# Optimization experiments

Measured on AMD Instinct MI355X. Metric: run time of the kernel, lower is better.

Reference implementation:

```python
import jax, jax.numpy as jnp
import numpy as np

N_STATE = 1024
N_HEAD = 16
B, S = 2, 2048
NEG = -1e9  # finite stand-in for -inf in the additive causal mask


def setup_inputs() -> dict:
    key = jax.random.key(0)
    ks = jax.random.split(key, 8)
    sd = N_STATE ** -0.5
    x = jax.random.normal(ks[0], (B, S, N_STATE), dtype=jnp.float32)
    # additive causal mask, as in Whisper: upper triangle = -inf
    i = jnp.arange(S)
    mask = jnp.where(i[None, :] > i[:, None], NEG, 0.0).astype(jnp.float32)
    return {
        "x": x,
        "mask": mask,
        "Wq": jax.random.normal(ks[1], (N_STATE, N_STATE), jnp.float32) * sd,
        "bq": jax.random.normal(ks[2], (N_STATE,), jnp.float32) * 0.02,
        "Wk": jax.random.normal(ks[3], (N_STATE, N_STATE), jnp.float32) * sd,
        "Wv": jax.random.normal(ks[4], (N_STATE, N_STATE), jnp.float32) * sd,
        "bv": jax.random.normal(ks[5], (N_STATE,), jnp.float32) * 0.02,
        "Wo": jax.random.normal(ks[6], (N_STATE, N_STATE), jnp.float32) * sd,
        "bo": jax.random.normal(ks[7], (N_STATE,), jnp.float32) * 0.02,
    }


def reference(x, mask, Wq, bq, Wk, Wv, bv, Wo, bo):
    B_, S_, D = x.shape
    H = N_HEAD
    hd = D // H
    scale = hd ** -0.25  # applied to both q and k, per the source

    q = (x @ Wq + bq).reshape(B_, S_, H, hd) * scale   # [B,S,H,hd]
    k = (x @ Wk).reshape(B_, S_, H, hd) * scale        # key has no bias
    v = (x @ Wv + bv).reshape(B_, S_, H, hd)

    qk = jnp.einsum("bqhd,bkhd->bhqk", q, k) + mask[:S_, :S_]
    w = jax.nn.softmax(qk.astype(jnp.float32), axis=-1).astype(q.dtype)
    o = jnp.einsum("bhqk,bkhd->bqhd", w, v).reshape(B_, S_, D)
    return o @ Wo + bo
```

## Files before the change

kernel.cpp:

```cpp
#include <hip/hip_runtime.h>
#include <hip/hip_bf16.h>

#define BB 2
#define SS 2048
#define DD 1024
#define HH 16
#define HD 64
#define QKSCALE 0.35355339059327373f
#define QKSCALE_E2 0.42466090144f
#define NEGBIG (-1e9f)

using u16 = unsigned short;
typedef __attribute__((ext_vector_type(8))) short short8;
typedef __attribute__((ext_vector_type(4))) float floatx4;
typedef __attribute__((ext_vector_type(4))) unsigned short ushort4v;

#define GLOBAL_AS __attribute__((address_space(1)))
#define LDS_AS __attribute__((address_space(3)))

__device__ __forceinline__ u16 f2b(float f) {
  union { float f; unsigned u; } v; v.f = f;
  return (u16)((v.u + 0x7fffu + ((v.u >> 16) & 1u)) >> 16);
}

__device__ __forceinline__ u16 bconv(float f) {
  union { __hip_bfloat16 h; u16 u; } cv;
  cv.h = __float2bfloat16(f);
  return cv.u;
}

__device__ __forceinline__ float ex2(float f) {
  return __builtin_amdgcn_exp2f(f);
}

__device__ __forceinline__ floatx4 vmax4(floatx4 a, floatx4 b) {
  return (floatx4){fmaxf(a[0], b[0]), fmaxf(a[1], b[1]),
                   fmaxf(a[2], b[2]), fmaxf(a[3], b[3])};
}

__device__ __forceinline__ void gload_lds16(const void* g, void* l) {
  __builtin_amdgcn_global_load_lds((GLOBAL_AS void*)(g), (LDS_AS void*)(l), 16, 0, 0);
}

__global__ __launch_bounds__(256) void cvt_bf16x4(const float4* __restrict__ src,
                                                  ushort4v* __restrict__ dst, int n4) {
  int i = blockIdx.x * 256 + threadIdx.x;
  if (i >= n4) return;
  float4 f = src[i];
  ushort4v o = { f2b(f.x), f2b(f.y), f2b(f.z), f2b(f.w) };
  dst[i] = o;
}

__global__ __launch_bounds__(256) void transpose_w(const float* __restrict__ s0,
                                                   const float* __restrict__ s1,
                                                   const float* __restrict__ s2,
                                                   const float* __restrict__ s3,
                                                   u16* __restrict__ dst) {
  __shared__ float tile[32][33];
  const float* src = (blockIdx.z == 0) ? s0 : (blockIdx.z == 1) ? s1
                   : (blockIdx.z == 2) ? s2 : s3;
  u16* d = dst + (size_t)blockIdx.z * 1024 * 1024;
  int c0 = blockIdx.x * 32, r0 = blockIdx.y * 32;
  int tx = threadIdx.x, ty = threadIdx.y;
#pragma unroll
  for (int i = 0; i < 4; ++i)
    tile[ty + i * 8][tx] = src[(size_t)(r0 + ty + i * 8) * 1024 + c0 + tx];
  __syncthreads();
#pragma unroll
  for (int i = 0; i < 4; ++i)
    d[(size_t)(c0 + ty + i * 8) * 1024 + r0 + tx] = f2b(tile[tx][ty + i * 8]);
}

template <typename OutT>
__global__ __launch_bounds__(256, 3)
void gemm_bt(const u16* __restrict__ A, const u16* __restrict__ Bt,
             OutT* __restrict__ C, const float* __restrict__ bias,
             float scale, int M, int N, int K) {
  const int tid = threadIdx.x;
  const int lane = tid & 63;
  const int w = tid >> 6;
  const int id = (int)blockIdx.x;
  const int swz = (id & 7) * 64 + (id >> 3);
  const int m0 = (swz & 63) * 64;
  const int n0 = (swz >> 6) * 128;
  __shared__ u16 As[2][64 * 64];
  __shared__ u16 Bs[2][128 * 64];
  floatx4 acc[2][4];
#pragma unroll
  for (int i = 0; i < 2; ++i)
#pragma unroll
    for (int j = 0; j < 4; ++j) acc[i][j] = (floatx4){0.f, 0.f, 0.f, 0.f};

  const int wr = (w >> 1) * 32;
  const int wc = (w & 1) * 64;
  const int g = lane >> 4;
  const int lr = lane & 15;
  const size_t strideA = (size_t)K * 2;

  auto stage = [&](int k0, int buf) {
#pragma unroll
    for (int p = 0; p < 2; ++p) {
      int L = tid * 16 + p * 4096;
      int row = L >> 7;
      int cb = (L ^ ((row & 7) << 4)) & 127;
      gload_lds16((const char*)A + (size_t)(m0 + row) * strideA + k0 * 2 + cb,
                  (char*)As[buf] + p * 4096 + w * 1024);
    }
#pragma unroll
    for (int p = 0; p < 4; ++p) {
      int L = tid * 16 + p * 4096;
      int row = L >> 7;
      int cb = (L ^ ((row & 7) << 4)) & 127;
      gload_lds16((const char*)Bt + (size_t)(n0 + row) * strideA + k0 * 2 + cb,
                  (char*)Bs[buf] + p * 4096 + w * 1024);
    }
  };

  const int nsteps = K >> 6;
  stage(0, 0);
  for (int t = 0; t < nsteps; ++t) {
    const int buf = t & 1;
    __syncthreads();
    if (t + 1 < nsteps) stage((t + 1) << 6, buf ^ 1);
    const u16* as = As[buf];
    const u16* bs = Bs[buf];
#pragma unroll
    for (int ks = 0; ks < 2; ++ks) {
      short8 af[2], bf[4];
      const int c0 = ks * 32 + g * 8;
#pragma unroll
      for (int mi = 0; mi < 2; ++mi) {
        int row = wr + mi * 16 + lr;
        af[mi] = *(const short8*)(as + row * 64 + (c0 ^ ((row & 7) << 3)));
      }
#pragma unroll
      for (int ni = 0; ni < 4; ++ni) {
        int row = wc + ni * 16 + lr;
        bf[ni] = *(const short8*)(bs + row * 64 + (c0 ^ ((row & 7) << 3)));
      }
      __builtin_amdgcn_s_setprio(1);
#pragma unroll
      for (int mi = 0; mi < 2; ++mi)
#pragma unroll
        for (int ni = 0; ni < 4; ++ni)
          acc[mi][ni] = __builtin_amdgcn_mfma_f32_16x16x32_bf16(af[mi], bf[ni],
                                                                acc[mi][ni], 0, 0, 0);
      __builtin_amdgcn_s_setprio(0);
    }
  }
#pragma unroll
  for (int ni = 0; ni < 4; ++ni) {
    int col = n0 + wc + ni * 16 + lr;
    float bvv = bias ? bias[col] : 0.f;
#pragma unroll
    for (int mi = 0; mi < 2; ++mi) {
#pragma unroll
      for (int r = 0; r < 4; ++r) {
        int rowg = m0 + wr + mi * 16 + g * 4 + r;
        float val = (acc[mi][ni][r] + bvv) * scale;
        if constexpr (sizeof(OutT) == 4) C[(size_t)rowg * N + col] = val;
        else C[(size_t)rowg * N + col] = (OutT)f2b(val);
      }
    }
  }
}

__global__ __launch_bounds__(256, 4)
void gemm_qkv(const u16* __restrict__ A, const u16* __restrict__ Wt3,
              u16* __restrict__ Out3, u16* __restrict__ Vt,
              const float* __restrict__ bq, const float* __restrict__ bv) {
  const int id = (int)blockIdx.x;
  const int swz = (id & 7) * 96 + (id >> 3);
  const int bx = swz & 31;
  const int rest = swz >> 5;
  const int by = rest & 7;
  const int seg = rest >> 3;
  const u16* Bt = Wt3 + (size_t)seg * 1024 * 1024;
  u16* C = Out3 + (size_t)seg * 4096 * 1024;
  const float* bias = (seg == 0) ? bq : (seg == 2) ? bv : nullptr;
  const float scale = (seg == 2) ? 1.0f : QKSCALE_E2;

  const int tid = threadIdx.x;
  const int lane = tid & 63;
  const int w = tid >> 6;
  const int m0 = bx * 128;
  const int n0 = by * 128;
  __shared__ u16 As[2][64 * 64];
  __shared__ u16 Bs[2][64 * 64];
  floatx4 acc[4][4];
#pragma unroll
  for (int i = 0; i < 4; ++i)
#pragma unroll
    for (int j = 0; j < 4; ++j) acc[i][j] = (floatx4){0.f, 0.f, 0.f, 0.f};
  const int wr = (w >> 1) * 64;
  const int wc = (w & 1) * 64;
  const int g = lane >> 4;
  const int lr = lane & 15;

  auto stage = [&](int k0, int buf) {
#pragma unroll
    for (int p = 0; p < 2; ++p) {
      int L = tid * 16 + p * 4096;
      int lrow = L >> 7;
      int un = (L & 127) ^ ((lrow & 7) << 4);
      int r = lrow * 2 + (un >> 6);
      int cb = un & 63;
      gload_lds16((const char*)A + (size_t)(m0 + r) * 2048 + k0 * 2 + cb,
                  (char*)As[buf] + p * 4096 + w * 1024);
      gload_lds16((const char*)Bt + (size_t)(n0 + r) * 2048 + k0 * 2 + cb,
                  (char*)Bs[buf] + p * 4096 + w * 1024);
    }
  };

  stage(0, 0);
  for (int t = 0; t < 32; ++t) {
    const int buf = t & 1;
    __syncthreads();
    if (t + 1 < 32) stage((t + 1) << 5, buf ^ 1);
    const u16* as = As[buf];
    const u16* bs = Bs[buf];
    short8 af[4], bf[4];
#pragma unroll
    for (int mi = 0; mi < 4; ++mi) {
      int r = wr + mi * 16 + lr;
      af[mi] = *(const short8*)((const char*)as +
               ((r >> 1) * 128 + ((((r & 1) << 6) | (g * 16)) ^ (((r >> 1) & 7) << 4))));
    }
#pragma unroll
    for (int ni = 0; ni < 4; ++ni) {
      int r = wc + ni * 16 + lr;
      bf[ni] = *(const short8*)((const char*)bs +
               ((r >> 1) * 128 + ((((r & 1) << 6) | (g * 16)) ^ (((r >> 1) & 7) << 4))));
    }
    __builtin_amdgcn_s_setprio(1);
#pragma unroll
    for (int mi = 0; mi < 4; ++mi)
#pragma unroll
      for (int ni = 0; ni < 4; ++ni)
        acc[mi][ni] = __builtin_amdgcn_mfma_f32_16x16x32_bf16(af[mi], bf[ni],
                                                              acc[mi][ni], 0, 0, 0);
    __builtin_amdgcn_s_setprio(0);
  }

  if (seg == 2) {
    const int bseg = m0 >> 11;
    const int s0 = (m0 & 2047) + wr + g * 4;
#pragma unroll
    for (int ni = 0; ni < 4; ++ni) {
      int d = n0 + wc + ni * 16 + lr;
      float bvv = bv[d];
      u16* vrow = Vt + (size_t)(bseg * 1024 + d) * 2048;
#pragma unroll
      for (int mi = 0; mi < 4; ++mi) {
        ushort4v pk = { f2b(acc[mi][ni][0] + bvv), f2b(acc[mi][ni][1] + bvv),
                        f2b(acc[mi][ni][2] + bvv), f2b(acc[mi][ni][3] + bvv) };
        *(ushort4v*)(vrow + s0 + mi * 16) = pk;
      }
    }
    return;
  }

  __syncthreads();
  u16* eb = (w == 0) ? (u16*)As[0] : (w == 1) ? (u16*)As[1]
          : (w == 2) ? (u16*)Bs[0] : (u16*)Bs[1];
  const int rr = lane >> 2;
  const int cc = lane & 3;
  float bv4[4];
#pragma unroll
  for (int ni = 0; ni < 4; ++ni)
    bv4[ni] = bias ? bias[n0 + wc + ni * 16 + lr] : 0.f;
#pragma unroll
  for (int mi = 0; mi < 4; ++mi) {
#pragma unroll
    for (int ni = 0; ni < 4; ++ni)
#pragma unroll
      for (int r = 0; r < 4; ++r)
        eb[(g * 4 + r) * 72 + ni * 16 + lr] =
            f2b((acc[mi][ni][r] + bv4[ni]) * scale);
    short8 v0 = *(const short8*)(eb + rr * 72 + cc * 16);
    short8 v1 = *(const short8*)(eb + rr * 72 + cc * 16 + 8);
    u16* dst = C + (size_t)(m0 + wr + mi * 16 + rr) * 1024 + n0 + wc + cc * 16;
    *(short8*)dst = v0;
    *(short8*)(dst + 8) = v1;
  }
}

__device__ __forceinline__ void stream_softmax(floatx4 (&sa)[4], float& m, float& l,
                                               floatx4 (&acc)[4], u16* pl,
                                               bool diag, int wlr, int g, int lr) {
  if (diag) {
#pragma unroll
    for (int ct = 0; ct < 4; ++ct)
#pragma unroll
      for (int r = 0; r < 4; ++r)
        if (ct * 16 + g * 4 + r > wlr) sa[ct][r] += NEGBIG;
  }
  floatx4 v = vmax4(vmax4(sa[0], sa[1]), vmax4(sa[2], sa[3]));
  float mx = fmaxf(fmaxf(v[0], v[1]), fmaxf(v[2], v[3]));
  mx = fmaxf(mx, __shfl_xor(mx, 16, 64));
  mx = fmaxf(mx, __shfl_xor(mx, 32, 64));
  if (!__all(mx <= m + 8.f)) {
    float mn = fmaxf(m, mx);
    float al = ex2(m - mn);
    l *= al;
#pragma unroll
    for (int dt = 0; dt < 4; ++dt) acc[dt] *= al;
    m = mn;
  }
  floatx4 p[4];
#pragma unroll
  for (int ct = 0; ct < 4; ++ct)
#pragma unroll
    for (int r = 0; r < 4; ++r)
      p[ct][r] = ex2(sa[ct][r] - m);
  floatx4 s = (p[0] + p[1]) + (p[2] + p[3]);
  float rs = (s[0] + s[1]) + (s[2] + s[3]);
  rs += __shfl_xor(rs, 16, 64);
  rs += __shfl_xor(rs, 32, 64);
  l += rs;
#pragma unroll
  for (int ct = 0; ct < 4; ++ct) {
    ushort4v pk = { bconv(p[ct][0]), bconv(p[ct][1]),
                    bconv(p[ct][2]), bconv(p[ct][3]) };
    *(ushort4v*)((char*)pl + ((lr * 128 + ct * 32 + g * 8) ^ ((lr & 7) << 4))) = pk;
  }
}

__global__ __launch_bounds__(256, 4)
void flash_attn(const u16* __restrict__ q, const u16* __restrict__ k,
                const u16* __restrict__ vt, u16* __restrict__ o) {
  const int tid = threadIdx.x;
  const int lane = tid & 63;
  const int w = tid >> 6;
  const int g = lane >> 4;
  const int lr = lane & 15;
  const int i = (int)blockIdx.x;
  const int x = i & 7;
  const int kk = i >> 3;
  const int s = kk & 3;
  const int mI = kk >> 2;
  const int u = mI >> 3;
  const int v = mI & 7;
  const int gg = x * 4 + s;
  const int b = gg >> 4;
  const int h = gg & 15;
  const int a = (u + s) & 3;
  const int qt = (a == 0) ? v : (a == 1) ? (31 - v) : (a == 2) ? (16 + v) : (15 - v);
  const int row0 = qt * 64 + w * 16;
  const int wlr = w * 16 + lr;

  __shared__ u16 Ks[2][64 * 64];
  __shared__ u16 Vs[2][64 * 64];
  __shared__ u16 Pl[4][16 * 64];

  short8 qf[2];
  {
    const u16* qp = q + (size_t)(b * SS + row0 + lr) * DD + h * HD + g * 8;
    qf[0] = *(const short8*)qp;
    qf[1] = *(const short8*)(qp + 32);
  }
  floatx4 acc[4];
#pragma unroll
  for (int dt = 0; dt < 4; ++dt) acc[dt] = (floatx4){0.f, 0.f, 0.f, 0.f};
  float m = -1e30f, l = 0.f;

  const char* kbase = (const char*)(k + (size_t)(b * SS) * DD + h * HD);
  const char* vbase = (const char*)(vt + (size_t)((b * HH + h) * HD) * SS);
  const int nt = qt + 1;

  auto stage = [&](int t, int buf) {
    const int kvb = t * 64;
#pragma unroll
    for (int p = 0; p < 2; ++p) {
      int L = tid * 16 + p * 4096;
      int row = L >> 7;
      int cb = (L ^ ((row & 7) << 4)) & 127;
      gload_lds16(kbase + (size_t)(kvb + row) * (DD * 2) + cb,
                  (char*)Ks + buf * 8192 + p * 4096 + w * 1024);
      gload_lds16(vbase + (size_t)row * (SS * 2) + kvb * 2 + cb,
                  (char*)Vs + buf * 8192 + p * 4096 + w * 1024);
    }
  };

  stage(0, 0);
  int cur = 0;
  for (int t = 0; t < nt; ++t) {
    __syncthreads();
    if (t + 1 < nt) stage(t + 1, cur ^ 1);
    const u16* kc = Ks[cur];
    const u16* vc = Vs[cur];

    floatx4 sa[4];
#pragma unroll
    for (int ct = 0; ct < 4; ++ct) sa[ct] = (floatx4){0.f, 0.f, 0.f, 0.f};
    __builtin_amdgcn_s_setprio(1);
#pragma unroll
    for (int ks = 0; ks < 2; ++ks) {
      const int c0 = ks * 32 + g * 8;
#pragma unroll
      for (int ct = 0; ct < 4; ++ct) {
        int row = ct * 16 + lr;
        short8 kf = *(const short8*)(kc + row * 64 + (c0 ^ ((row & 7) << 3)));
        sa[ct] = __builtin_amdgcn_mfma_f32_16x16x32_bf16(kf, qf[ks], sa[ct], 0, 0, 0);
      }
    }
    __builtin_amdgcn_s_setprio(0);

    stream_softmax(sa, m, l, acc, Pl[w], t == qt, wlr, g, lr);

    __builtin_amdgcn_s_setprio(1);
#pragma unroll
    for (int ks = 0; ks < 2; ++ks) {
      const int c0 = ks * 32 + g * 8;
      int pby = (lr * 128 + ks * 64 + g * 16) ^ ((lr & 7) << 4);
      short8 pf = *(const short8*)((const char*)Pl[w] + pby);
#pragma unroll
      for (int dt = 0; dt < 4; ++dt) {
        int row = dt * 16 + lr;
        short8 vf = *(const short8*)(vc + row * 64 + (c0 ^ ((row & 7) << 3)));
        acc[dt] = __builtin_amdgcn_mfma_f32_16x16x32_bf16(vf, pf, acc[dt], 0, 0, 0);
      }
    }
    __builtin_amdgcn_s_setprio(0);
    cur ^= 1;
  }

  float inv = 1.0f / l;
#pragma unroll
  for (int dt = 0; dt < 4; ++dt) {
    ushort4v pa = { bconv(acc[dt][0] * inv), bconv(acc[dt][1] * inv),
                    bconv(acc[dt][2] * inv), bconv(acc[dt][3] * inv) };
    *(ushort4v*)(o + (size_t)(b * SS + row0 + lr) * DD + h * HD + dt * 16 + g * 4) = pa;
  }
}

extern "C" void kernel_launch(void* const* d_in, const int* in_sizes, int n_in,
                              void* d_out, int out_size, void* d_ws, size_t ws_size,
                              hipStream_t stream) {
  const float* x  = (const float*)d_in[0];
  const float* Wq = (const float*)d_in[2];
  const float* bq = (const float*)d_in[3];
  const float* Wk = (const float*)d_in[4];
  const float* Wv = (const float*)d_in[5];
  const float* bv = (const float*)d_in[6];
  const float* Wo = (const float*)d_in[7];
  const float* bo = (const float*)d_in[8];
  float* out = (float*)d_out;

  char* ws = (char*)d_ws;
  u16* xb  = (u16*)(ws);
  u16* wt  = (u16*)(ws + (8u << 20));
  u16* qkv = (u16*)(ws + (16u << 20));
  u16* vtb = (u16*)(ws + (40u << 20));
  u16* ob  = (u16*)(ws + (48u << 20));
  u16* wot = wt + 3u * 1024 * 1024;

  dim3 tb(32, 8);
  cvt_bf16x4<<<4096, 256, 0, stream>>>((const float4*)x, (ushort4v*)xb,
                                       (BB * SS * DD) / 4);
  transpose_w<<<dim3(32, 32, 4), tb, 0, stream>>>(Wq, Wk, Wv, Wo, wt);
  gemm_qkv<<<768, 256, 0, stream>>>(xb, wt, qkv, vtb, bq, bv);
  flash_attn<<<1024, 256, 0, stream>>>(qkv, qkv + (size_t)4096 * 1024, vtb, ob);
  gemm_bt<float><<<512, 256, 0, stream>>>(ob, wot, out, bo, 1.0f,
                                          4096, 1024, 1024);
}
```

Before: 109.5 us.

## Pair mirrored causal query tiles per block to share K/V staging

New measurement: 123.3 us. 1.13x slower.

```diff
diff --git a/kernel.cpp b/kernel.cpp
--- a/kernel.cpp
+++ b/kernel.cpp
@@ -326,7 +326,7 @@
   }
 }
 
-__global__ __launch_bounds__(256, 4)
+__global__ __launch_bounds__(256, 3)
 void flash_attn(const u16* __restrict__ q, const u16* __restrict__ k,
                 const u16* __restrict__ vt, u16* __restrict__ o) {
   const int tid = threadIdx.x;
@@ -334,51 +334,55 @@
   const int w = tid >> 6;
   const int g = lane >> 4;
   const int lr = lane & 15;
-  const int i = (int)blockIdx.x;
-  const int x = i & 7;
-  const int kk = i >> 3;
-  const int s = kk & 3;
-  const int mI = kk >> 2;
-  const int u = mI >> 3;
-  const int v = mI & 7;
-  const int gg = x * 4 + s;
-  const int b = gg >> 4;
-  const int h = gg & 15;
-  const int a = (u + s) & 3;
-  const int qt = (a == 0) ? v : (a == 1) ? (31 - v) : (a == 2) ? (16 + v) : (15 - v);
-  const int row0 = qt * 64 + w * 16;
+  const int id = (int)blockIdx.x;
+  const int x = id & 7;
+  const int rest = id >> 3;
+  const int s = rest & 3;
+  const int p = rest >> 2;
+  const int head = x * 4 + s;
+  const int b = head >> 4;
+  const int h = head & 15;
+  const int qtA = p, qtB = 31 - p;
+  const int rowA = qtA * 64 + w * 16;
+  const int rowB = qtB * 64 + w * 16;
   const int wlr = w * 16 + lr;
 
   __shared__ u16 Ks[2][64 * 64];
   __shared__ u16 Vs[2][64 * 64];
-  __shared__ u16 Pl[4][16 * 64];
-
-  short8 qf[2];
+  __shared__ u16 Pl[4][2][16 * 64];
+
+  short8 qfA[2], qfB[2];
   {
-    const u16* qp = q + (size_t)(b * SS + row0 + lr) * DD + h * HD + g * 8;
-    qf[0] = *(const short8*)qp;
-    qf[1] = *(const short8*)(qp + 32);
-  }
-  floatx4 acc[4];
-#pragma unroll
-  for (int dt = 0; dt < 4; ++dt) acc[dt] = (floatx4){0.f, 0.f, 0.f, 0.f};
-  float m = -1e30f, l = 0.f;
+    const u16* qa = q + (size_t)(b * SS + rowA + lr) * DD + h * HD + g * 8;
+    qfA[0] = *(const short8*)qa;
+    qfA[1] = *(const short8*)(qa + 32);
+    const u16* qb = q + (size_t)(b * SS + rowB + lr) * DD + h * HD + g * 8;
+    qfB[0] = *(const short8*)qb;
+    qfB[1] = *(const short8*)(qb + 32);
+  }
+  floatx4 accA[4], accB[4];
+#pragma unroll
+  for (int dt = 0; dt < 4; ++dt) {
+    accA[dt] = (floatx4){0.f, 0.f, 0.f, 0.f};
+    accB[dt] = (floatx4){0.f, 0.f, 0.f, 0.f};
+  }
+  float mA = -1e30f, lA = 0.f, mB = -1e30f, lB = 0.f;
 
   const char* kbase = (const char*)(k + (size_t)(b * SS) * DD + h * HD);
   const char* vbase = (const char*)(vt + (size_t)((b * HH + h) * HD) * SS);
-  const int nt = qt + 1;
+  const int nt = qtB + 1;
 
   auto stage = [&](int t, int buf) {
     const int kvb = t * 64;
 #pragma unroll
-    for (int p = 0; p < 2; ++p) {
-      int L = tid * 16 + p * 4096;
+    for (int pp = 0; pp < 2; ++pp) {
+      int L = tid * 16 + pp * 4096;
       int row = L >> 7;
       int cb = (L ^ ((row & 7) << 4)) & 127;
       gload_lds16(kbase + (size_t)(kvb + row) * (DD * 2) + cb,
-                  (char*)Ks + buf * 8192 + p * 4096 + w * 1024);
+                  (char*)Ks + buf * 8192 + pp * 4096 + w * 1024);
       gload_lds16(vbase + (size_t)row * (SS * 2) + kvb * 2 + cb,
-                  (char*)Vs + buf * 8192 + p * 4096 + w * 1024);
+                  (char*)Vs + buf * 8192 + pp * 4096 + w * 1024);
     }
   };
 
@@ -389,10 +393,14 @@
     if (t + 1 < nt) stage(t + 1, cur ^ 1);
     const u16* kc = Ks[cur];
     const u16* vc = Vs[cur];
-
-    floatx4 sa[4];
-#pragma unroll
-    for (int ct = 0; ct < 4; ++ct) sa[ct] = (floatx4){0.f, 0.f, 0.f, 0.f};
+    const bool actA = (t <= qtA);
+
+    floatx4 saA[4], saB[4];
+#pragma unroll
+    for (int ct = 0; ct < 4; ++ct) {
+      saA[ct] = (floatx4){0.f, 0.f, 0.f, 0.f};
+      saB[ct] = (floatx4){0.f, 0.f, 0.f, 0.f};
+    }
     __builtin_amdgcn_s_setprio(1);
 #pragma unroll
     for (int ks = 0; ks < 2; ++ks) {
@@ -401,36 +409,48 @@
       for (int ct = 0; ct < 4; ++ct) {
         int row = ct * 16 + lr;
         short8 kf = *(const short8*)(kc + row * 64 + (c0 ^ ((row & 7) << 3)));
-        sa[ct] = __builtin_amdgcn_mfma_f32_16x16x32_bf16(kf, qf[ks], sa[ct], 0, 0, 0);
+        saB[ct] = __builtin_amdgcn_mfma_f32_16x16x32_bf16(kf, qfB[ks], saB[ct], 0, 0, 0);
+        if (actA)
+          saA[ct] = __builtin_amdgcn_mfma_f32_16x16x32_bf16(kf, qfA[ks], saA[ct], 0, 0, 0);
       }
     }
     __builtin_amdgcn_s_setprio(0);
 
-    stream_softmax(sa, m, l, acc, Pl[w], t == qt, wlr, g, lr);
+    if (actA)
+      stream_softmax(saA, mA, lA, accA, Pl[w][0], t == qtA, wlr, g, lr);
+    stream_softmax(saB, mB, lB, accB, Pl[w][1], t == qtB, wlr, g, lr);
 
     __builtin_amdgcn_s_setprio(1);
 #pragma unroll
     for (int ks = 0; ks < 2; ++ks) {
       const int c0 = ks * 32 + g * 8;
       int pby = (lr * 128 + ks * 64 + g * 16) ^ ((lr & 7) << 4);
-      short8 pf = *(const short8*)((const char*)Pl[w] + pby);
+      short8 pfB = *(const short8*)((const char*)Pl[w][1] + pby);
+      short8 pfA = pfB;
+      if (actA) pfA = *(const short8*)((const char*)Pl[w][0] + pby);
 #pragma unroll
       for (int dt = 0; dt < 4; ++dt) {
         int row = dt * 16 + lr;
         short8 vf = *(const short8*)(vc + row * 64 + (c0 ^ ((row & 7) << 3)));
-        acc[dt] = __builtin_amdgcn_mfma_f32_16x16x32_bf16(vf, pf, acc[dt], 0, 0, 0);
+        accB[dt] = __builtin_amdgcn_mfma_f32_16x16x32_bf16(vf, pfB, accB[dt], 0, 0, 0);
+        if (actA)
+          accA[dt] = __builtin_amdgcn_mfma_f32_16x16x32_bf16(vf, pfA, accA[dt], 0, 0, 0);
       }
     }
     __builtin_amdgcn_s_setprio(0);
     cur ^= 1;
   }
 
-  float inv = 1.0f / l;
+  float invA = 1.0f / lA;
+  float invB = 1.0f / lB;
 #pragma unroll
   for (int dt = 0; dt < 4; ++dt) {
-    ushort4v pa = { bconv(acc[dt][0] * inv), bconv(acc[dt][1] * inv),
-                    bconv(acc[dt][2] * inv), bconv(acc[dt][3] * inv) };
-    *(ushort4v*)(o + (size_t)(b * SS + row0 + lr) * DD + h * HD + dt * 16 + g * 4) = pa;
+    ushort4v pa = { bconv(accA[dt][0] * invA), bconv(accA[dt][1] * invA),
+                    bconv(accA[dt][2] * invA), bconv(accA[dt][3] * invA) };
+    ushort4v pb = { bconv(accB[dt][0] * invB), bconv(accB[dt][1] * invB),
+                    bconv(accB[dt][2] * invB), bconv(accB[dt][3] * invB) };
+    *(ushort4v*)(o + (size_t)(b * SS + rowA + lr) * DD + h * HD + dt * 16 + g * 4) = pa;
+    *(ushort4v*)(o + (size_t)(b * SS + rowB + lr) * DD + h * HD + dt * 16 + g * 4) = pb;
   }
 }
 
@@ -460,7 +480,7 @@
                                        (BB * SS * DD) / 4);
   transpose_w<<<dim3(32, 32, 4), tb, 0, stream>>>(Wq, Wk, Wv, Wo, wt);
   gemm_qkv<<<768, 256, 0, stream>>>(xb, wt, qkv, vtb, bq, bv);
-  flash_attn<<<1024, 256, 0, stream>>>(qkv, qkv + (size_t)4096 * 1024, vtb, ob);
+  flash_attn<<<512, 256, 0, stream>>>(qkv, qkv + (size_t)4096 * 1024, vtb, ob);
   gemm_bt<float><<<512, 256, 0, stream>>>(ob, wot, out, bo, 1.0f,
                                           4096, 1024, 1024);
 }
```

## Shrink QKV GEMM tile to 64x128 with BK=64 and double the grid

Applied to the files above, without the earlier changes.

After: 114.1 us. 1.04x slower.

```diff
diff --git a/kernel.cpp b/kernel.cpp
--- a/kernel.cpp
+++ b/kernel.cpp
@@ -165,34 +165,31 @@
   }
 }
 
-__global__ __launch_bounds__(256, 4)
+__global__ __launch_bounds__(256, 3)
 void gemm_qkv(const u16* __restrict__ A, const u16* __restrict__ Wt3,
               u16* __restrict__ Out3, u16* __restrict__ Vt,
               const float* __restrict__ bq, const float* __restrict__ bv) {
-  const int id = (int)blockIdx.x;
-  const int swz = (id & 7) * 96 + (id >> 3);
-  const int bx = swz & 31;
-  const int rest = swz >> 5;
-  const int by = rest & 7;
-  const int seg = rest >> 3;
-  const u16* Bt = Wt3 + (size_t)seg * 1024 * 1024;
-  u16* C = Out3 + (size_t)seg * 4096 * 1024;
-  const float* bias = (seg == 0) ? bq : (seg == 2) ? bv : nullptr;
-  const float scale = (seg == 2) ? 1.0f : QKSCALE_E2;
-
   const int tid = threadIdx.x;
   const int lane = tid & 63;
   const int w = tid >> 6;
-  const int m0 = bx * 128;
-  const int n0 = by * 128;
+  const int id = (int)blockIdx.x;
+  const int swz = (id & 7) * 192 + (id >> 3);
+  const int seg = swz >> 9;
+  const int r2 = swz & 511;
+  const int m0 = (r2 & 63) * 64;
+  const int n0 = (r2 >> 6) * 128;
+  const u16* Bt = Wt3 + (size_t)seg * 1024 * 1024;
+  u16* C = Out3 + (size_t)seg * 4096 * 1024;
+
   __shared__ u16 As[2][64 * 64];
-  __shared__ u16 Bs[2][64 * 64];
-  floatx4 acc[4][4];
-#pragma unroll
-  for (int i = 0; i < 4; ++i)
+  __shared__ u16 Bs[2][128 * 64];
+  floatx4 acc[2][4];
+#pragma unroll
+  for (int i = 0; i < 2; ++i)
 #pragma unroll
     for (int j = 0; j < 4; ++j) acc[i][j] = (floatx4){0.f, 0.f, 0.f, 0.f};
-  const int wr = (w >> 1) * 64;
+
+  const int wr = (w >> 1) * 32;
   const int wc = (w & 1) * 64;
   const int g = lane >> 4;
   const int lr = lane & 15;
@@ -201,45 +198,51 @@
 #pragma unroll
     for (int p = 0; p < 2; ++p) {
       int L = tid * 16 + p * 4096;
-      int lrow = L >> 7;
-      int un = (L & 127) ^ ((lrow & 7) << 4);
-      int r = lrow * 2 + (un >> 6);
-      int cb = un & 63;
-      gload_lds16((const char*)A + (size_t)(m0 + r) * 2048 + k0 * 2 + cb,
+      int row = L >> 7;
+      int cb = (L ^ ((row & 7) << 4)) & 127;
+      gload_lds16((const char*)A + (size_t)(m0 + row) * 2048 + k0 * 2 + cb,
                   (char*)As[buf] + p * 4096 + w * 1024);
-      gload_lds16((const char*)Bt + (size_t)(n0 + r) * 2048 + k0 * 2 + cb,
+    }
+#pragma unroll
+    for (int p = 0; p < 4; ++p) {
+      int L = tid * 16 + p * 4096;
+      int row = L >> 7;
+      int cb = (L ^ ((row & 7) << 4)) & 127;
+      gload_lds16((const char*)Bt + (size_t)(n0 + row) * 2048 + k0 * 2 + cb,
                   (char*)Bs[buf] + p * 4096 + w * 1024);
     }
   };
 
   stage(0, 0);
-  for (int t = 0; t < 32; ++t) {
+  for (int t = 0; t < 16; ++t) {
     const int buf = t & 1;
     __syncthreads();
-    if (t + 1 < 32) stage((t + 1) << 5, buf ^ 1);
+    if (t + 1 < 16) stage((t + 1) << 6, buf ^ 1);
     const u16* as = As[buf];
     const u16* bs = Bs[buf];
-    short8 af[4], bf[4];
-#pragma unroll
-    for (int mi = 0; mi < 4; ++mi) {
-      int r = wr + mi * 16 + lr;
-      af[mi] = *(const short8*)((const char*)as +
-               ((r >> 1) * 128 + ((((r & 1) << 6) | (g * 16)) ^ (((r >> 1) & 7) << 4))));
-    }
-#pragma unroll
-    for (int ni = 0; ni < 4; ++ni) {
-      int r = wc + ni * 16 + lr;
-      bf[ni] = *(const short8*)((const char*)bs +
-               ((r >> 1) * 128 + ((((r & 1) << 6) | (g * 16)) ^ (((r >> 1) & 7) << 4))));
-    }
-    __builtin_amdgcn_s_setprio(1);
-#pragma unroll
-    for (int mi = 0; mi < 4; ++mi)
-#pragma unroll
-      for (int ni = 0; ni < 4; ++ni)
-        acc[mi][ni] = __builtin_amdgcn_mfma_f32_16x16x32_bf16(af[mi], bf[ni],
-                                                              acc[mi][ni], 0, 0, 0);
-    __builtin_amdgcn_s_setprio(0);
+#pragma unroll
+    for (int ks = 0; ks < 2; ++ks) {
+      short8 af[2], bf[4];
+      const int c0 = ks * 32 + g * 8;
+#pragma unroll
+      for (int mi = 0; mi < 2; ++mi) {
+        int row = wr + mi * 16 + lr;
+        af[mi] = *(const short8*)(as + row * 64 + (c0 ^ ((row & 7) << 3)));
+      }
+#pragma unroll
+      for (int ni = 0; ni < 4; ++ni) {
+        int row = wc + ni * 16 + lr;
+        bf[ni] = *(const short8*)(bs + row * 64 + (c0 ^ ((row & 7) << 3)));
+      }
+      __builtin_amdgcn_s_setprio(1);
+#pragma unroll
+      for (int mi = 0; mi < 2; ++mi)
+#pragma unroll
+        for (int ni = 0; ni < 4; ++ni)
+          acc[mi][ni] = __builtin_amdgcn_mfma_f32_16x16x32_bf16(af[mi], bf[ni],
+                                                                acc[mi][ni], 0, 0, 0);
+      __builtin_amdgcn_s_setprio(0);
+    }
   }
 
   if (seg == 2) {
@@ -251,7 +254,7 @@
       float bvv = bv[d];
       u16* vrow = Vt + (size_t)(bseg * 1024 + d) * 2048;
 #pragma unroll
-      for (int mi = 0; mi < 4; ++mi) {
+      for (int mi = 0; mi < 2; ++mi) {
         ushort4v pk = { f2b(acc[mi][ni][0] + bvv), f2b(acc[mi][ni][1] + bvv),
                         f2b(acc[mi][ni][2] + bvv), f2b(acc[mi][ni][3] + bvv) };
         *(ushort4v*)(vrow + s0 + mi * 16) = pk;
@@ -261,27 +264,27 @@
   }
 
   __syncthreads();
-  u16* eb = (w == 0) ? (u16*)As[0] : (w == 1) ? (u16*)As[1]
-          : (w == 2) ? (u16*)Bs[0] : (u16*)Bs[1];
-  const int rr = lane >> 2;
-  const int cc = lane & 3;
+  u16* eb = (u16*)As + w * 1152;
+  const float scale = QKSCALE_E2;
   float bv4[4];
 #pragma unroll
   for (int ni = 0; ni < 4; ++ni)
-    bv4[ni] = bias ? bias[n0 + wc + ni * 16 + lr] : 0.f;
-#pragma unroll
-  for (int mi = 0; mi < 4; ++mi) {
+    bv4[ni] = (seg == 0) ? bq[n0 + wc + ni * 16 + lr] : 0.f;
+#pragma unroll
+  for (int mi = 0; mi < 2; ++mi) {
 #pragma unroll
     for (int ni = 0; ni < 4; ++ni)
 #pragma unroll
       for (int r = 0; r < 4; ++r)
         eb[(g * 4 + r) * 72 + ni * 16 + lr] =
             f2b((acc[mi][ni][r] + bv4[ni]) * scale);
-    short8 v0 = *(const short8*)(eb + rr * 72 + cc * 16);
-    short8 v1 = *(const short8*)(eb + rr * 72 + cc * 16 + 8);
-    u16* dst = C + (size_t)(m0 + wr + mi * 16 + rr) * 1024 + n0 + wc + cc * 16;
-    *(short8*)dst = v0;
-    *(short8*)(dst + 8) = v1;
+#pragma unroll
+    for (int jj = 0; jj < 2; ++jj) {
+      int row = (lane >> 3) + jj * 8;
+      int ch = lane & 7;
+      short8 vv = *(const short8*)(eb + row * 72 + ch * 8);
+      *(short8*)(C + (size_t)(m0 + wr + mi * 16 + row) * 1024 + n0 + wc + ch * 8) = vv;
+    }
   }
 }
 
@@ -459,7 +462,7 @@
   cvt_bf16x4<<<4096, 256, 0, stream>>>((const float4*)x, (ushort4v*)xb,
                                        (BB * SS * DD) / 4);
   transpose_w<<<dim3(32, 32, 4), tb, 0, stream>>>(Wq, Wk, Wv, Wo, wt);
-  gemm_qkv<<<768, 256, 0, stream>>>(xb, wt, qkv, vtb, bq, bv);
+  gemm_qkv<<<1536, 256, 0, stream>>>(xb, wt, qkv, vtb, bq, bv);
   flash_attn<<<1024, 256, 0, stream>>>(qkv, qkv + (size_t)4096 * 1024, vtb, ob);
   gemm_bt<float><<<512, 256, 0, stream>>>(ob, wot, out, bo, 1.0f,
                                           4096, 1024, 1024);
```
